# Optimization experiments

Measured on AMD Instinct MI355X. Metric: run time of the kernel, lower is better.

## Reference

```python
import jax, jax.numpy as jnp
import numpy as np
from jax import lax

B, T, D, H, K = 2, 2048, 1024, 16, 4
HD = D // H           # head dim = 64
CONV_DIM = 3 * D      # q + k + v channels


def _l2norm(x, eps=1e-6):
    return x * lax.rsqrt(jnp.sum(x * x, axis=-1, keepdims=True) + eps)


def setup_inputs() -> dict:
    key = jax.random.key(0)
    ks = jax.random.split(key, 8)
    s = 0.02
    return {
        "x": jax.random.normal(ks[0], (B, T, D), jnp.float32),
        "W_qkv": jax.random.normal(ks[1], (CONV_DIM, D), jnp.float32) * s,
        "conv_w": jax.random.normal(ks[2], (CONV_DIM, 1, K), jnp.float32) * 0.25,
        "W_z": jax.random.normal(ks[3], (D, D), jnp.float32) * s,
        "W_b": jax.random.normal(ks[4], (H, D), jnp.float32) * s,
        "W_a": jax.random.normal(ks[5], (H, D), jnp.float32) * s,
        "dt_bias": jnp.ones((H,), jnp.float32),
        "A_log": jnp.log(jnp.arange(1, H + 1, dtype=jnp.float32)),
        "W_out": jax.random.normal(ks[6], (D, D), jnp.float32) * s,
    }


def _forward(x, W_qkv, conv_w, W_z, W_b, W_a, dt_bias, A_log, W_out):
    b_, t_, d_ = x.shape
    # fused qkv projection: [B,T,3D]
    mixed = jnp.einsum("btd,cd->btc", x, W_qkv)
    # causal depthwise conv1d (left pad K-1, truncate to T)
    c = mixed.transpose(0, 2, 1)  # [B,3D,T]
    c = lax.conv_general_dilated(
        c, conv_w, window_strides=(1,), padding=[(K - 1, 0)],
        dimension_numbers=("NCH", "OIH", "NCH"), feature_group_count=CONV_DIM)
    mixed = jax.nn.silu(c).transpose(0, 2, 1)  # [B,T,3D]

    q, k, v = jnp.split(mixed, [d_, 2 * d_], axis=-1)
    q = q.reshape(b_, t_, H, HD)
    k = k.reshape(b_, t_, H, HD)
    v = v.reshape(b_, t_, H, HD)

    z = jnp.einsum("btd,ed->bte", x, W_z).reshape(b_, t_, H, HD)
    beta = jax.nn.sigmoid(jnp.einsum("btd,hd->bth", x, W_b))          # [B,T,H]
    g = -jnp.exp(A_log) * jax.nn.softplus(
        jnp.einsum("btd,hd->bth", x, W_a) + dt_bias)                   # [B,T,H]

    q = _l2norm(q) * (HD ** -0.5)
    k = _l2norm(k)

    # sequential gated delta-rule scan over time
    qs = q.transpose(1, 0, 2, 3)       # [T,B,H,HD]
    ks_ = k.transpose(1, 0, 2, 3)
    vs = v.transpose(1, 0, 2, 3)
    bs = beta.transpose(1, 0, 2)       # [T,B,H]
    gs = g.transpose(1, 0, 2)

    def step(S, inp):
        q_t, k_t, v_t, b_t, g_t = inp
        S = S * jnp.exp(g_t)[..., None, None]                         # decay state
        S = S + jnp.einsum("bhd,bhv->bhdv", k_t, v_t * b_t[..., None])  # rank-1 update
        o_t = jnp.einsum("bhd,bhdv->bhv", q_t, S)
        return S, o_t

    S0 = jnp.zeros((b_, H, HD, HD), x.dtype)
    _, out = lax.scan(step, S0, (qs, ks_, vs, bs, gs))                 # out: [T,B,H,HD]
    out = out.transpose(1, 0, 2, 3)                                    # [B,T,H,HD]

    # gated RMSNorm over head dim, gate = silu(z)
    var = jnp.mean(out * out, axis=-1, keepdims=True)
    out = out * lax.rsqrt(var + 1e-6) * jax.nn.silu(z)

    out = out.reshape(b_, t_, d_)
    return jnp.einsum("btd,ed->bte", out, W_out)


def reference(x, W_qkv, conv_w, W_z, W_b, W_a, dt_bias, A_log, W_out):
    return _forward(x, W_qkv, conv_w, W_z, W_b, W_a, dt_bias, A_log, W_out)
```

## Files before the change

### kernel.cpp

```cpp
#include <hip/hip_runtime.h>
#include <math.h>

#define B_  2
#define T_  2048
#define D_  1024
#define H_  16
#define HD_ 64
#define CD_ 3072
#define L_  64
#define NC_ 32
#define TS  72
#define TT  8

typedef __attribute__((ext_vector_type(8))) short bf16x8;
typedef __attribute__((ext_vector_type(4))) float f32x4;
typedef __attribute__((ext_vector_type(4))) unsigned short u16x4;

__device__ __forceinline__ unsigned short f2bf(float f) {
    unsigned int u = __float_as_uint(f);
    unsigned int r = (u + 0x7fffu + ((u >> 16) & 1u)) >> 16;
    return (unsigned short)r;
}
__device__ __forceinline__ float bf2f(unsigned short u) {
    return __uint_as_float(((unsigned int)u) << 16);
}

__global__ __launch_bounds__(256)
void cvt_all(const float* __restrict__ x, const float* __restrict__ Wqkv,
             const float* __restrict__ Wz, const float* __restrict__ Wout,
             unsigned short* __restrict__ xb, unsigned short* __restrict__ Wqkvb,
             unsigned short* __restrict__ Wzb, unsigned short* __restrict__ Woutb) {
    int i = blockIdx.x * 256 + threadIdx.x;
    const float* src; unsigned short* dst; int li;
    if (i < 1048576)      { src = x;    dst = xb;    li = i; }
    else if (i < 1835008) { src = Wqkv; dst = Wqkvb; li = i - 1048576; }
    else if (i < 2097152) { src = Wz;   dst = Wzb;   li = i - 1835008; }
    else                  { src = Wout; dst = Woutb; li = i - 2097152; }
    float4 a = ((const float4*)src)[li];
    u16x4 o;
    o.x = f2bf(a.x); o.y = f2bf(a.y); o.z = f2bf(a.z); o.w = f2bf(a.w);
    ((u16x4*)dst)[li] = o;
}

__global__ __launch_bounds__(256)
void gemm_qkvz(const unsigned short* __restrict__ A,
               const unsigned short* __restrict__ Bw,
               unsigned short* __restrict__ mixedb, unsigned short* __restrict__ zb) {
    const int K = 1024;
    __shared__ short As[2][128 * 32];
    __shared__ short Bs[2][128 * 32];
    const int tid = threadIdx.x;
    const int wgid = blockIdx.x;
    const int bm = (wgid >> 5) * 128;
    const int bn = (wgid & 31) * 128;
    const int wave = tid >> 6;
    const int lane = tid & 63;
    const int wm = (wave >> 1) * 64;
    const int wn = (wave & 1) * 64;
    const int lr = lane & 15;
    const int lk = lane >> 4;

    f32x4 acc[4][4] = {};

    const int srow = tid >> 2;
    const int scol = (tid & 3) << 3;
    const unsigned short* Ag = A + (size_t)(bm + srow) * K + scol;
    const unsigned short* Bg = Bw + (size_t)(bn + srow) * K + scol;

#define STAGE_Q(buf, k0)                                                          \
    do {                                                                          \
        __builtin_amdgcn_global_load_lds(                                         \
            (const __attribute__((address_space(1))) void*)(Ag + (k0)),           \
            (__attribute__((address_space(3))) void*)(&As[buf][tid * 8]), 16, 0, 0); \
        __builtin_amdgcn_global_load_lds(                                         \
            (const __attribute__((address_space(1))) void*)(Ag + (size_t)64 * K + (k0)), \
            (__attribute__((address_space(3))) void*)(&As[buf][tid * 8 + 2048]), 16, 0, 0); \
        __builtin_amdgcn_global_load_lds(                                         \
            (const __attribute__((address_space(1))) void*)(Bg + (k0)),           \
            (__attribute__((address_space(3))) void*)(&Bs[buf][tid * 8]), 16, 0, 0); \
        __builtin_amdgcn_global_load_lds(                                         \
            (const __attribute__((address_space(1))) void*)(Bg + (size_t)64 * K + (k0)), \
            (__attribute__((address_space(3))) void*)(&Bs[buf][tid * 8 + 2048]), 16, 0, 0); \
    } while (0)

#define COMPUTE_Q(buf)                                                            \
    do {                                                                          \
        const short* pA = &As[buf][(wm + lr) * 32 + lk * 8];                      \
        const short* pB = &Bs[buf][(wn + lr) * 32 + lk * 8];                      \
        bf16x8 a[4], b[4];                                                        \
        _Pragma("unroll")                                                         \
        for (int mi = 0; mi < 4; ++mi) a[mi] = *(const bf16x8*)(pA + mi * 16 * 32); \
        _Pragma("unroll")                                                         \
        for (int ni = 0; ni < 4; ++ni) b[ni] = *(const bf16x8*)(pB + ni * 16 * 32); \
        _Pragma("unroll")                                                         \
        for (int mi = 0; mi < 4; ++mi)                                            \
            _Pragma("unroll")                                                     \
            for (int ni = 0; ni < 4; ++ni)                                        \
                acc[mi][ni] = __builtin_amdgcn_mfma_f32_16x16x32_bf16(            \
                    a[mi], b[ni], acc[mi][ni], 0, 0, 0);                          \
    } while (0)

    STAGE_Q(0, 0);
    __syncthreads();
    int cur = 0;
    for (int it = 0; it < 31; ++it) {
        STAGE_Q(cur ^ 1, (it + 1) * 32);
        COMPUTE_Q(cur);
        __syncthreads();
        cur ^= 1;
    }
    COMPUTE_Q(cur);

    const int r0 = lk * 4;
#pragma unroll
    for (int mi = 0; mi < 4; ++mi)
#pragma unroll
        for (int ni = 0; ni < 4; ++ni) {
            int row = bm + wm + mi * 16 + r0;
            int ncol = bn + wn + ni * 16 + lr;
            if (ncol < 3072) {
                unsigned short* cp = mixedb + (size_t)row * 3072 + ncol;
#pragma unroll
                for (int r = 0; r < 4; ++r)
                    cp[(size_t)r * 3072] = f2bf(acc[mi][ni][r]);
            } else {
                unsigned short* cp = zb + (size_t)row * 1024 + (ncol - 3072);
#pragma unroll
                for (int r = 0; r < 4; ++r)
                    cp[(size_t)r * 1024] = f2bf(acc[mi][ni][r]);
            }
        }
}

__global__ __launch_bounds__(256)
void gemm_out(const unsigned short* __restrict__ A,
              const unsigned short* __restrict__ Bw,
              float* __restrict__ C) {
    const int K = 1024, N = 1024;
    __shared__ short As[2][128 * 32];
    __shared__ short Bs[2][128 * 32];
    const int tid = threadIdx.x;
    const int wgid = blockIdx.x;
    const int bm = (wgid >> 3) * 128;
    const int bn = (wgid & 7) * 128;
    const int wave = tid >> 6;
    const int lane = tid & 63;
    const int wm = (wave >> 1) * 64;
    const int wn = (wave & 1) * 64;
    const int lr = lane & 15;
    const int lk = lane >> 4;

    f32x4 acc[4][4] = {};

    const int srow = tid >> 2;
    const int scol = (tid & 3) << 3;
    const unsigned short* Ag = A + (size_t)(bm + srow) * K + scol;
    const unsigned short* Bg = Bw + (size_t)(bn + srow) * K + scol;

    STAGE_Q(0, 0);
    __syncthreads();
    int cur = 0;
    for (int it = 0; it < 31; ++it) {
        STAGE_Q(cur ^ 1, (it + 1) * 32);
        COMPUTE_Q(cur);
        __syncthreads();
        cur ^= 1;
    }
    COMPUTE_Q(cur);

    const int r0 = lk * 4;
#pragma unroll
    for (int mi = 0; mi < 4; ++mi)
#pragma unroll
        for (int ni = 0; ni < 4; ++ni) {
            float* cp = C + (size_t)(bm + wm + mi * 16 + r0) * N + bn + wn + ni * 16 + lr;
#pragma unroll
            for (int r = 0; r < 4; ++r)
                cp[(size_t)r * N] = acc[mi][ni][r];
        }
}

#define PJS 129
__global__ __launch_bounds__(256)
void proj_bg_partial(const float* __restrict__ x, const float* __restrict__ Wb,
                     const float* __restrict__ Wa, float* __restrict__ partial) {
    const int m0 = (blockIdx.x >> 3) * 32;
    const int ks = blockIdx.x & 7;
    const int k0 = ks * 128;
    const int tid = threadIdx.x;
    __shared__ float xs[32 * PJS];
    __shared__ float wsh[32 * PJS];
    const int sr = tid >> 3;
    const int sc = (tid & 7) << 4;
    const int mi2 = tid >> 3;
    const int n02 = (tid & 7) << 2;

    {
        const float* xrow = x + (size_t)(m0 + sr) * D_ + k0 + sc;
        const float* wrow = ((sr < 16) ? (Wb + (size_t)sr * D_) : (Wa + (size_t)(sr - 16) * D_)) + k0 + sc;
#pragma unroll
        for (int j = 0; j < 16; j += 4) {
            float4 a = *(const float4*)(xrow + j);
            float4 b = *(const float4*)(wrow + j);
            xs[sr * PJS + sc + j + 0] = a.x; xs[sr * PJS + sc + j + 1] = a.y;
            xs[sr * PJS + sc + j + 2] = a.z; xs[sr * PJS + sc + j + 3] = a.w;
            wsh[sr * PJS + sc + j + 0] = b.x; wsh[sr * PJS + sc + j + 1] = b.y;
            wsh[sr * PJS + sc + j + 2] = b.z; wsh[sr * PJS + sc + j + 3] = b.w;
        }
    }
    __syncthreads();

    float acc[4] = {0.f, 0.f, 0.f, 0.f};
#pragma unroll 8
    for (int kk = 0; kk < 128; ++kk) {
        float av = xs[mi2 * PJS + kk];
#pragma unroll
        for (int j = 0; j < 4; ++j)
            acc[j] = fmaf(av, wsh[(n02 + j) * PJS + kk], acc[j]);
    }
    float* op = partial + (size_t)ks * (4096 * 32) + (size_t)(m0 + mi2) * 32 + n02;
    *(float4*)op = make_float4(acc[0], acc[1], acc[2], acc[3]);
}

__global__ __launch_bounds__(256)
void proj_bg_reduce(const float* __restrict__ partial, const float* __restrict__ dt_bias,
                    const float* __restrict__ A_log,
                    float* __restrict__ beta, float* __restrict__ g) {
    const int gid = blockIdx.x * 256 + threadIdx.x;
    const int m = gid >> 5;
    const int n = gid & 31;
    float s = 0.f;
#pragma unroll
    for (int ks = 0; ks < 8; ++ks)
        s += partial[(size_t)ks * (4096 * 32) + gid];
    if (n < 16) {
        beta[(size_t)m * H_ + n] = 1.f / (1.f + expf(-s));
    } else {
        int h = n - 16;
        float spin = s + dt_bias[h];
        float sp = (spin > 20.f) ? spin : log1pf(expf(spin));
        g[(size_t)m * H_ + h] = -expf(A_log[h]) * sp;
    }
}

__global__ __launch_bounds__(256)
void conv_silu_tt(const unsigned short* __restrict__ mixedb,
                  const float* __restrict__ conv_w,
                  unsigned short* __restrict__ qkvb) {
    int idx = blockIdx.x * 256 + threadIdx.x;
    const int cq = idx % (CD_ / 4);
    const int bt8 = idx / (CD_ / 4);
    const int t0 = (bt8 % (T_ / TT)) * TT;
    const int b = bt8 / (T_ / TT);
    const int c0 = cq << 2;
    const unsigned short* base = mixedb + (size_t)(b * T_ + t0) * CD_ + c0;

    float vals[TT + 3][4];
#pragma unroll
    for (int i = 0; i < TT + 3; ++i) {
        int t = t0 + i - 3;
        if (t >= 0) {
            u16x4 m = *(const u16x4*)(base + (ptrdiff_t)(i - 3) * CD_);
            vals[i][0] = bf2f(m.x); vals[i][1] = bf2f(m.y);
            vals[i][2] = bf2f(m.z); vals[i][3] = bf2f(m.w);
        } else {
            vals[i][0] = vals[i][1] = vals[i][2] = vals[i][3] = 0.f;
        }
    }
    const float4* wp = (const float4*)(conv_w + (size_t)c0 * 4);
    float4 w[4] = {wp[0], wp[1], wp[2], wp[3]};

    unsigned short* outp = qkvb + (size_t)(b * T_ + t0) * CD_ + c0;
#pragma unroll
    for (int tt = 0; tt < TT; ++tt) {
        u16x4 r;
        float s0 = vals[tt + 3][0] * w[0].w + vals[tt + 2][0] * w[0].z
                 + vals[tt + 1][0] * w[0].y + vals[tt + 0][0] * w[0].x;
        float s1 = vals[tt + 3][1] * w[1].w + vals[tt + 2][1] * w[1].z
                 + vals[tt + 1][1] * w[1].y + vals[tt + 0][1] * w[1].x;
        float s2 = vals[tt + 3][2] * w[2].w + vals[tt + 2][2] * w[2].z
                 + vals[tt + 1][2] * w[2].y + vals[tt + 0][2] * w[2].x;
        float s3 = vals[tt + 3][3] * w[3].w + vals[tt + 2][3] * w[3].z
                 + vals[tt + 1][3] * w[3].y + vals[tt + 0][3] * w[3].x;
        r.x = f2bf(s0 / (1.f + expf(-s0)));
        r.y = f2bf(s1 / (1.f + expf(-s1)));
        r.z = f2bf(s2 / (1.f + expf(-s2)));
        r.w = f2bf(s3 / (1.f + expf(-s3)));
        *(u16x4*)(outp + (size_t)tt * CD_) = r;
    }
}

__global__ __launch_bounds__(256)
void chunk_phase1(const unsigned short* __restrict__ qkvb,
                  const float* __restrict__ beta, const float* __restrict__ gg,
                  float* __restrict__ dST, float* __restrict__ cum,
                  float* __restrict__ ac) {
    const int cid = blockIdx.x;
    const int c = cid & (NC_ - 1);
    const int bh = cid >> 5;
    const int b = bh >> 4, h = bh & 15;
    const int tid = threadIdx.x;
    const int wave = tid >> 6, lane = tid & 63;
    const int t0 = c * L_;

    __shared__ __align__(16) short kT[64 * TS];
    __shared__ __align__(16) short vT[64 * TS];
    __shared__ float cumS[64], wS[64];
    __shared__ float ksumP[4][64];

    const unsigned short* rowp = qkvb + (size_t)(b * T_ + t0 + lane) * CD_ + h * HD_ + wave * 16;
    bf16x8 k0 = *(const bf16x8*)(rowp + D_);
    bf16x8 k1 = *(const bf16x8*)(rowp + D_ + 8);
    bf16x8 v0 = *(const bf16x8*)(rowp + 2 * D_);
    bf16x8 v1 = *(const bf16x8*)(rowp + 2 * D_ + 8);

    {
        float ks = 0.f;
#pragma unroll
        for (int j = 0; j < 8; ++j) {
            float a = bf2f((unsigned short)k0[j]); ks = fmaf(a, a, ks);
            float bq = bf2f((unsigned short)k1[j]); ks = fmaf(bq, bq, ks);
        }
        ksumP[wave][lane] = ks;
    }

    if (wave == 0) {
        float s = gg[(size_t)(b * T_ + t0 + lane) * H_ + h];
#pragma unroll
        for (int off = 1; off < 64; off <<= 1) {
            float up = __shfl_up(s, off, 64);
            if (lane >= off) s += up;
        }
        cumS[lane] = s;
        float cend = __shfl(s, 63, 64);
        wS[lane] = expf(cend - s) * beta[(size_t)(b * T_ + t0 + lane) * H_ + h];
        cum[(size_t)bh * T_ + t0 + lane] = s;
        if (lane == 63) ac[cid] = expf(cend);
    }
    __syncthreads();
    const float kn = rsqrtf(ksumP[0][lane] + ksumP[1][lane] + ksumP[2][lane]
                            + ksumP[3][lane] + 1e-6f);
    const float w = wS[lane] * kn;
#pragma unroll
    for (int j = 0; j < 8; ++j) {
        kT[(wave * 16 + j) * TS + lane] = k0[j];
        kT[(wave * 16 + 8 + j) * TS + lane] = k1[j];
        vT[(wave * 16 + j) * TS + lane] = f2bf(bf2f((unsigned short)v0[j]) * w);
        vT[(wave * 16 + 8 + j) * TS + lane] = f2bf(bf2f((unsigned short)v1[j]) * w);
    }
    __syncthreads();

    const int lr = lane & 15, lk = lane >> 4;
    f32x4 acc[4] = {};
    const short* pA = vT + (wave * 16 + lr) * TS + lk * 8;
#pragma unroll
    for (int kk = 0; kk < 2; ++kk) {
        bf16x8 a = *(const bf16x8*)(pA + kk * 32);
#pragma unroll
        for (int n = 0; n < 4; ++n) {
            bf16x8 bfr = *(const bf16x8*)(kT + (n * 16 + lr) * TS + lk * 8 + kk * 32);
            acc[n] = __builtin_amdgcn_mfma_f32_16x16x32_bf16(a, bfr, acc[n], 0, 0, 0);
        }
    }
#pragma unroll
    for (int n = 0; n < 4; ++n) {
        float* op = dST + (size_t)cid * 4096 + (wave * 16 + lk * 4) * 64 + n * 16 + lr;
#pragma unroll
        for (int r = 0; r < 4; ++r)
            op[r * 64] = acc[n][r];
    }
}

__global__ __launch_bounds__(256)
void chunk_phase2(float* __restrict__ dST, const float* __restrict__ ac) {
    const int gid = blockIdx.x * 256 + threadIdx.x;
    const int bh = gid >> 12;
    const int e = gid & 4095;
    float s = 0.f;
    for (int c = 0; c < NC_; ++c) {
        size_t off = (size_t)(bh * NC_ + c) * 4096 + e;
        float tmp = dST[off];
        dST[off] = s;
        s = fmaf(ac[bh * NC_ + c], s, tmp);
    }
}

__global__ __launch_bounds__(256)
void chunk_phase3(const unsigned short* __restrict__ qkvb,
                  const float* __restrict__ beta, const float* __restrict__ cum,
                  const float* __restrict__ states,
                  const unsigned short* __restrict__ zb,
                  unsigned short* __restrict__ normb) {
    const int cid = blockIdx.x;
    const int c = cid & (NC_ - 1);
    const int bh = cid >> 5;
    const int b = bh >> 4, h = bh & 15;
    const int tid = threadIdx.x;
    const int wave = tid >> 6, lane = tid & 63;
    const int t0 = c * L_;

    __shared__ __align__(16) short vT[64 * TS];
    __shared__ __align__(16) short sT[64 * TS];
    __shared__ __align__(16) short pS[64 * TS];
    __shared__ float cumS[64], betaS[64];
    __shared__ float invq[64], invk[64];

    {
        const unsigned short* rowp = qkvb + (size_t)(b * T_ + t0 + lane) * CD_ + 2 * D_ + h * HD_ + wave * 16;
        bf16x8 v0 = *(const bf16x8*)rowp;
        bf16x8 v1 = *(const bf16x8*)(rowp + 8);
#pragma unroll
        for (int j = 0; j < 8; ++j) {
            vT[(wave * 16 + j) * TS + lane] = v0[j];
            vT[(wave * 16 + 8 + j) * TS + lane] = v1[j];
        }
    }
    {
        const float* sp = states + (size_t)cid * 4096 + (tid >> 2) * 64 + (tid & 3) * 16;
        short* dp = sT + (tid >> 2) * TS + (tid & 3) * 16;
#pragma unroll
        for (int j = 0; j < 16; j += 4) {
            float4 f = *(const float4*)(sp + j);
            dp[j] = f2bf(f.x); dp[j + 1] = f2bf(f.y);
            dp[j + 2] = f2bf(f.z); dp[j + 3] = f2bf(f.w);
        }
    }
    {
        int row = tid >> 2;
        int seg = (tid & 3) << 4;
        const unsigned short* qr = qkvb + (size_t)(b * T_ + t0 + row) * CD_ + h * HD_ + seg;
        bf16x8 a0 = *(const bf16x8*)qr;
        bf16x8 a1 = *(const bf16x8*)(qr + 8);
        float sq = 0.f;
#pragma unroll
        for (int j = 0; j < 8; ++j) {
            float v = bf2f((unsigned short)a0[j]); sq = fmaf(v, v, sq);
            v = bf2f((unsigned short)a1[j]); sq = fmaf(v, v, sq);
        }
        sq += __shfl_xor(sq, 1, 64);
        sq += __shfl_xor(sq, 2, 64);
        const unsigned short* kr = qr + D_;
        bf16x8 b0 = *(const bf16x8*)kr;
        bf16x8 b1 = *(const bf16x8*)(kr + 8);
        float sk = 0.f;
#pragma unroll
        for (int j = 0; j < 8; ++j) {
            float v = bf2f((unsigned short)b0[j]); sk = fmaf(v, v, sk);
            v = bf2f((unsigned short)b1[j]); sk = fmaf(v, v, sk);
        }
        sk += __shfl_xor(sk, 1, 64);
        sk += __shfl_xor(sk, 2, 64);
        if ((tid & 3) == 0) {
            invq[row] = 0.125f * rsqrtf(sq + 1e-6f);
            invk[row] = rsqrtf(sk + 1e-6f);
        }
    }
    if (tid < 64) {
        cumS[tid] = cum[(size_t)bh * T_ + t0 + tid];
        betaS[tid] = beta[(size_t)(b * T_ + t0 + tid) * H_ + h];
    }
    __syncthreads();

    const int lr = lane & 15, lk = lane >> 4;
    const unsigned short* qrow = qkvb + (size_t)(b * T_ + t0 + wave * 16 + lr) * CD_ + h * HD_;
    bf16x8 qf0 = *(const bf16x8*)(qrow + lk * 8);
    bf16x8 qf1 = *(const bf16x8*)(qrow + 32 + lk * 8);

    f32x4 pacc[4] = {};
#pragma unroll
    for (int n = 0; n < 4; ++n) {
        const unsigned short* krow = qkvb + (size_t)(b * T_ + t0 + n * 16 + lr) * CD_ + D_ + h * HD_;
        bf16x8 b0 = *(const bf16x8*)(krow + lk * 8);
        bf16x8 b1 = *(const bf16x8*)(krow + 32 + lk * 8);
        pacc[n] = __builtin_amdgcn_mfma_f32_16x16x32_bf16(qf0, b0, pacc[n], 0, 0, 0);
        pacc[n] = __builtin_amdgcn_mfma_f32_16x16x32_bf16(qf1, b1, pacc[n], 0, 0, 0);
    }
#pragma unroll
    for (int n = 0; n < 4; ++n) {
        int s = n * 16 + lr;
        float cs = cumS[s], bsk = betaS[s] * invk[s];
#pragma unroll
        for (int r = 0; r < 4; ++r) {
            int t = wave * 16 + lk * 4 + r;
            float pv = (s <= t) ? expf(cumS[t] - cs) * bsk * pacc[n][r] * invq[t] : 0.f;
            pS[t * TS + s] = f2bf(pv);
        }
    }
    __syncthreads();

    f32x4 oacc[4] = {};
#pragma unroll
    for (int n = 0; n < 4; ++n) {
        const short* srow = sT + (n * 16 + lr) * TS + lk * 8;
        bf16x8 b0 = *(const bf16x8*)srow;
        bf16x8 b1 = *(const bf16x8*)(srow + 32);
        oacc[n] = __builtin_amdgcn_mfma_f32_16x16x32_bf16(qf0, b0, oacc[n], 0, 0, 0);
        oacc[n] = __builtin_amdgcn_mfma_f32_16x16x32_bf16(qf1, b1, oacc[n], 0, 0, 0);
    }
    float qsc[4];
#pragma unroll
    for (int r = 0; r < 4; ++r) {
        int t = wave * 16 + lk * 4 + r;
        qsc[r] = expf(cumS[t]) * invq[t];
    }
#pragma unroll
    for (int n = 0; n < 4; ++n)
#pragma unroll
        for (int r = 0; r < 4; ++r) oacc[n][r] *= qsc[r];
    const short* prow = pS + (wave * 16 + lr) * TS + lk * 8;
    bf16x8 pf0 = *(const bf16x8*)prow;
    bf16x8 pf1 = *(const bf16x8*)(prow + 32);
#pragma unroll
    for (int n = 0; n < 4; ++n) {
        const short* vrow = vT + (n * 16 + lr) * TS + lk * 8;
        bf16x8 b0 = *(const bf16x8*)vrow;
        bf16x8 b1 = *(const bf16x8*)(vrow + 32);
        oacc[n] = __builtin_amdgcn_mfma_f32_16x16x32_bf16(pf0, b0, oacc[n], 0, 0, 0);
        oacc[n] = __builtin_amdgcn_mfma_f32_16x16x32_bf16(pf1, b1, oacc[n], 0, 0, 0);
    }

#pragma unroll
    for (int r = 0; r < 4; ++r) {
        int t = wave * 16 + lk * 4 + r;
        float ss = 0.f;
#pragma unroll
        for (int n = 0; n < 4; ++n) ss = fmaf(oacc[n][r], oacc[n][r], ss);
        ss += __shfl_xor(ss, 1, 64);
        ss += __shfl_xor(ss, 2, 64);
        ss += __shfl_xor(ss, 4, 64);
        ss += __shfl_xor(ss, 8, 64);
        float inv = rsqrtf(ss * (1.f / 64.f) + 1e-6f);
        size_t rowoff = (size_t)(b * T_ + t0 + t) * D_ + h * HD_;
#pragma unroll
        for (int n = 0; n < 4; ++n) {
            float zv = bf2f(zb[rowoff + n * 16 + lr]);
            float sz = zv / (1.f + expf(-zv));
            normb[rowoff + n * 16 + lr] = f2bf(oacc[n][r] * inv * sz);
        }
    }
}

extern "C" void kernel_launch(void* const* d_in, const int* in_sizes, int n_in,
                              void* d_out, int out_size, void* d_ws, size_t ws_size,
                              hipStream_t stream) {
    const float* x       = (const float*)d_in[0];
    const float* W_qkv   = (const float*)d_in[1];
    const float* conv_w  = (const float*)d_in[2];
    const float* W_z     = (const float*)d_in[3];
    const float* W_b     = (const float*)d_in[4];
    const float* W_a     = (const float*)d_in[5];
    const float* dt_bias = (const float*)d_in[6];
    const float* A_log   = (const float*)d_in[7];
    const float* W_out   = (const float*)d_in[8];
    float* out = (float*)d_out;

    float* ws = (float*)d_ws;
    unsigned short* mixedb = (unsigned short*)ws;
    float* dST    = ws;
    unsigned short* normb = (unsigned short*)(ws + 4194304);
    float* betab  = ws + 8388608;
    float* gb     = ws + 8454144;
    float* cum    = ws + 8519680;
    float* ac     = ws + 8585216;
    unsigned short* Woutb = (unsigned short*)(ws + 8586240);
    unsigned short* xb    = (unsigned short*)(ws + 12582912);
    unsigned short* Wqkvb = (unsigned short*)(ws + 14680064);
    unsigned short* Wzb   = (unsigned short*)(ws + 16252928);
    unsigned short* qkvb  = (unsigned short*)(ws + 12582912);
    unsigned short* zb    = (unsigned short*)(ws + 18874368);
    float* bgpart = ws + 23068672;

    const int M = B_ * T_;
    dim3 blk(256);

    cvt_all<<<dim3(9216), blk, 0, stream>>>(x, W_qkv, W_z, W_out, xb, Wqkvb, Wzb, Woutb);

    gemm_qkvz<<<dim3(1024), blk, 0, stream>>>(xb, Wqkvb, mixedb, zb);

    conv_silu_tt<<<dim3(B_ * (T_ / TT) * (CD_ / 4) / 256), blk, 0, stream>>>(mixedb, conv_w, qkvb);

    proj_bg_partial<<<dim3(1024), blk, 0, stream>>>(x, W_b, W_a, bgpart);
    proj_bg_reduce<<<dim3(512), blk, 0, stream>>>(bgpart, dt_bias, A_log, betab, gb);

    chunk_phase1<<<dim3(B_ * H_ * NC_), blk, 0, stream>>>(qkvb, betab, gb, dST, cum, ac);
    chunk_phase2<<<dim3(B_ * H_ * 4096 / 256), blk, 0, stream>>>(dST, ac);
    chunk_phase3<<<dim3(B_ * H_ * NC_), blk, 0, stream>>>(qkvb, betab, cum, dST, zb, normb);

    gemm_out<<<dim3(256), blk, 0, stream>>>(normb, Woutb, out);
}
```

Measured before the change: 164.6 us.

## Replace QKV/Z projection GEMM with 256x256-tile, 512-thread swizzled-LDS kernel

The fused qkv+z projection GEMM is rewritten from 128x128 tiles with 256 threads and K-steps of 32 into 256x256 tiles with 8 waves, K-steps of 64, and 128 KB of dynamic LDS. LDS chunks use an XOR swizzle to avoid bank conflicts, and s_setprio is raised around the MFMA bursts. The goal is more operand reuse per byte loaded and fewer global loads per FLOP. In exchange, only one workgroup fits per CU, the grid shrinks to 256 blocks, and register pressure rises with 32 accumulators per wave.

```diff
diff --git a/kernel.cpp b/kernel.cpp
--- a/kernel.cpp
+++ b/kernel.cpp
@@ -42,17 +42,117 @@
     ((u16x4*)dst)[li] = o;
 }
 
-__global__ __launch_bounds__(256)
-void gemm_qkvz(const unsigned short* __restrict__ A,
-               const unsigned short* __restrict__ Bw,
-               unsigned short* __restrict__ mixedb, unsigned short* __restrict__ zb) {
+__global__ __launch_bounds__(512, 2)
+void gemm_qkvz256(const unsigned short* __restrict__ A,
+                  const unsigned short* __restrict__ Bw,
+                  unsigned short* __restrict__ mixedb, unsigned short* __restrict__ zb) {
     const int K = 1024;
+    extern __shared__ short lds[];
+    const int tid = threadIdx.x;
+    const int bm = (blockIdx.x >> 4) * 256;
+    const int bn = (blockIdx.x & 15) * 256;
+    const int wid = tid >> 6;
+    const int lane = tid & 63;
+    const int wm = (wid >> 2) * 128;
+    const int wn = (wid & 3) * 64;
+    const int lr = lane & 15;
+    const int lk = lane >> 4;
+
+    f32x4 acc[8][4] = {};
+
+    const int srow = tid >> 3;
+    const int sphys = tid & 7;
+    const int sgcol = ((sphys ^ (srow & 7)) << 3);
+    const unsigned short* Ag = A + (size_t)(bm + srow) * K + sgcol;
+    const unsigned short* Bg = Bw + (size_t)(bn + srow) * K + sgcol;
+    short* ldsAd = lds + srow * 64 + sphys * 8;
+    short* ldsBd = ldsAd + 16384;
+
+#define STG256(bsel, kt)                                                         \
+    do {                                                                         \
+        _Pragma("unroll")                                                        \
+        for (int j = 0; j < 4; ++j) {                                            \
+            __builtin_amdgcn_global_load_lds(                                    \
+                (const __attribute__((address_space(1))) void*)(Ag + (size_t)(j * 64) * K + (kt) * 64), \
+                (__attribute__((address_space(3))) void*)(ldsAd + (bsel) * 32768 + j * 4096), 16, 0, 0); \
+            __builtin_amdgcn_global_load_lds(                                    \
+                (const __attribute__((address_space(1))) void*)(Bg + (size_t)(j * 64) * K + (kt) * 64), \
+                (__attribute__((address_space(3))) void*)(ldsBd + (bsel) * 32768 + j * 4096), 16, 0, 0); \
+        }                                                                        \
+    } while (0)
+
+#define CMP256(bsel)                                                             \
+    do {                                                                         \
+        const short* LA = lds + (bsel) * 32768 + (wm + lr) * 64;                 \
+        const short* LB = lds + (bsel) * 32768 + 16384 + (wn + lr) * 64;         \
+        _Pragma("unroll")                                                        \
+        for (int ks = 0; ks < 2; ++ks) {                                         \
+            const int ch = ((ks * 4 + lk) ^ (lr & 7)) * 8;                       \
+            bf16x8 bf[4], af[4];                                                 \
+            _Pragma("unroll")                                                    \
+            for (int ni = 0; ni < 4; ++ni) bf[ni] = *(const bf16x8*)(LB + ni * 1024 + ch); \
+            _Pragma("unroll")                                                    \
+            for (int mi = 0; mi < 4; ++mi) af[mi] = *(const bf16x8*)(LA + mi * 1024 + ch); \
+            __builtin_amdgcn_s_setprio(1);                                       \
+            _Pragma("unroll")                                                    \
+            for (int mi = 0; mi < 4; ++mi)                                       \
+                _Pragma("unroll")                                                \
+                for (int ni = 0; ni < 4; ++ni)                                   \
+                    acc[mi][ni] = __builtin_amdgcn_mfma_f32_16x16x32_bf16(       \
+                        af[mi], bf[ni], acc[mi][ni], 0, 0, 0);                   \
+            __builtin_amdgcn_s_setprio(0);                                       \
+            _Pragma("unroll")                                                    \
+            for (int mi = 0; mi < 4; ++mi) af[mi] = *(const bf16x8*)(LA + (mi + 4) * 1024 + ch); \
+            __builtin_amdgcn_s_setprio(1);                                       \
+            _Pragma("unroll")                                                    \
+            for (int mi = 0; mi < 4; ++mi)                                       \
+                _Pragma("unroll")                                                \
+                for (int ni = 0; ni < 4; ++ni)                                   \
+                    acc[mi + 4][ni] = __builtin_amdgcn_mfma_f32_16x16x32_bf16(   \
+                        af[mi], bf[ni], acc[mi + 4][ni], 0, 0, 0);               \
+            __builtin_amdgcn_s_setprio(0);                                       \
+        }                                                                        \
+    } while (0)
+
+    STG256(0, 0);
+    __syncthreads();
+    for (int kt = 0; kt < 15; ++kt) {
+        STG256((kt + 1) & 1, kt + 1);
+        CMP256(kt & 1);
+        __syncthreads();
+    }
+    CMP256(1);
+
+    const int r0 = lk * 4;
+#pragma unroll
+    for (int mi = 0; mi < 8; ++mi)
+#pragma unroll
+        for (int ni = 0; ni < 4; ++ni) {
+            int row = bm + wm + mi * 16 + r0;
+            int col = bn + wn + ni * 16 + lr;
+            if (bn < 3072) {
+                unsigned short* cp = mixedb + (size_t)row * 3072 + col;
+#pragma unroll
+                for (int r = 0; r < 4; ++r) cp[(size_t)r * 3072] = f2bf(acc[mi][ni][r]);
+            } else {
+                unsigned short* cp = zb + (size_t)row * 1024 + (col - 3072);
+#pragma unroll
+                for (int r = 0; r < 4; ++r) cp[(size_t)r * 1024] = f2bf(acc[mi][ni][r]);
+            }
+        }
+}
+
+__global__ __launch_bounds__(256)
+void gemm_out(const unsigned short* __restrict__ A,
+              const unsigned short* __restrict__ Bw,
+              float* __restrict__ C) {
+    const int K = 1024, N = 1024;
     __shared__ short As[2][128 * 32];
     __shared__ short Bs[2][128 * 32];
     const int tid = threadIdx.x;
     const int wgid = blockIdx.x;
-    const int bm = (wgid >> 5) * 128;
-    const int bn = (wgid & 31) * 128;
+    const int bm = (wgid >> 3) * 128;
+    const int bn = (wgid & 7) * 128;
     const int wave = tid >> 6;
     const int lane = tid & 63;
     const int wm = (wave >> 1) * 64;
@@ -116,63 +216,6 @@
     for (int mi = 0; mi < 4; ++mi)
 #pragma unroll
         for (int ni = 0; ni < 4; ++ni) {
-            int row = bm + wm + mi * 16 + r0;
-            int ncol = bn + wn + ni * 16 + lr;
-            if (ncol < 3072) {
-                unsigned short* cp = mixedb + (size_t)row * 3072 + ncol;
-#pragma unroll
-                for (int r = 0; r < 4; ++r)
-                    cp[(size_t)r * 3072] = f2bf(acc[mi][ni][r]);
-            } else {
-                unsigned short* cp = zb + (size_t)row * 1024 + (ncol - 3072);
-#pragma unroll
-                for (int r = 0; r < 4; ++r)
-                    cp[(size_t)r * 1024] = f2bf(acc[mi][ni][r]);
-            }
-        }
-}
-
-__global__ __launch_bounds__(256)
-void gemm_out(const unsigned short* __restrict__ A,
-              const unsigned short* __restrict__ Bw,
-              float* __restrict__ C) {
-    const int K = 1024, N = 1024;
-    __shared__ short As[2][128 * 32];
-    __shared__ short Bs[2][128 * 32];
-    const int tid = threadIdx.x;
-    const int wgid = blockIdx.x;
-    const int bm = (wgid >> 3) * 128;
-    const int bn = (wgid & 7) * 128;
-    const int wave = tid >> 6;
-    const int lane = tid & 63;
-    const int wm = (wave >> 1) * 64;
-    const int wn = (wave & 1) * 64;
-    const int lr = lane & 15;
-    const int lk = lane >> 4;
-
-    f32x4 acc[4][4] = {};
-
-    const int srow = tid >> 2;
-    const int scol = (tid & 3) << 3;
-    const unsigned short* Ag = A + (size_t)(bm + srow) * K + scol;
-    const unsigned short* Bg = Bw + (size_t)(bn + srow) * K + scol;
-
-    STAGE_Q(0, 0);
-    __syncthreads();
-    int cur = 0;
-    for (int it = 0; it < 31; ++it) {
-        STAGE_Q(cur ^ 1, (it + 1) * 32);
-        COMPUTE_Q(cur);
-        __syncthreads();
-        cur ^= 1;
-    }
-    COMPUTE_Q(cur);
-
-    const int r0 = lk * 4;
-#pragma unroll
-    for (int mi = 0; mi < 4; ++mi)
-#pragma unroll
-        for (int ni = 0; ni < 4; ++ni) {
             float* cp = C + (size_t)(bm + wm + mi * 16 + r0) * N + bn + wn + ni * 16 + lr;
 #pragma unroll
             for (int r = 0; r < 4; ++r)
@@ -575,7 +618,7 @@
 
     cvt_all<<<dim3(9216), blk, 0, stream>>>(x, W_qkv, W_z, W_out, xb, Wqkvb, Wzb, Woutb);
 
-    gemm_qkvz<<<dim3(1024), blk, 0, stream>>>(xb, Wqkvb, mixedb, zb);
+    gemm_qkvz256<<<dim3(256), dim3(512), 131072, stream>>>(xb, Wqkvb, mixedb, zb);
 
     conv_silu_tt<<<dim3(B_ * (T_ / TT) * (CD_ / 4) / 256), blk, 0, stream>>>(mixedb, conv_w, qkvb);
 
```

Result: faster. 144.9 us (-12.0%).
